# Kernel optimization log

Measured on AMD Instinct MI355X. Metric: run time of the kernel, lower is better.

Reference implementation:

```python
import jax, jax.numpy as jnp
import numpy as np

B, S, H = 2, 2048, 1024
E, K, I = 8, 2, 512
NSH = 2
IS = I * NSH           # shared-expert intermediate = moe_inter * n_shared_experts
NUM_TASKS = 3
TEMP = 1.0             # router_temperature_init (eval: no annealing, no noise)


def setup_inputs() -> dict:
    key = jax.random.key(0)
    ks = jax.random.split(key, 11)
    s_h = 1.0 / np.sqrt(H).astype(np.float32)
    s_i = 1.0 / np.sqrt(I).astype(np.float32)
    s_is = 1.0 / np.sqrt(IS).astype(np.float32)
    return {
        "hidden_states": jax.random.normal(ks[0], (B, S, H), jnp.float32),
        "task_id": 1,
        "gate_w": jax.random.normal(ks[1], (E, H), jnp.float32) * s_h,
        "task_emb": jax.random.normal(ks[2], (NUM_TASKS, H), jnp.float32) * 0.02,
        "We_gate": jax.random.normal(ks[3], (E, H, I), jnp.float32) * s_h,
        "We_up": jax.random.normal(ks[4], (E, H, I), jnp.float32) * s_h,
        "We_down": jax.random.normal(ks[5], (E, I, H), jnp.float32) * s_i,
        "Ws_gate": jax.random.normal(ks[6], (H, IS), jnp.float32) * s_h,
        "Ws_up": jax.random.normal(ks[7], (H, IS), jnp.float32) * s_h,
        "Ws_down": jax.random.normal(ks[8], (IS, H), jnp.float32) * s_is,
        "Wc": jax.random.normal(ks[9], (H, 2), jnp.float32) * s_h,
    }


def _gelu(x):
    return jax.nn.gelu(x, approximate=False)  # matches torch F.gelu default (erf)


def reference(hidden_states, task_id, gate_w, task_emb, We_gate, We_up, We_down,
              Ws_gate, Ws_up, Ws_down, Wc):
    b, s, h = hidden_states.shape
    flat = hidden_states.reshape(-1, h)            # [T, H]
    T = flat.shape[0]

    # ---- NoisyTopKGating (eval: no gumbel noise, no dropout, no aux loss) ----
    gate_in = flat + task_emb[task_id]             # task-conditioned router input
    logits = (gate_in @ gate_w.T) / TEMP           # [T, E]
    scores = jax.nn.softmax(logits, axis=-1)
    topk_w, topk_idx = jax.lax.top_k(scores, K)    # [T, K]
    topk_w = topk_w / (topk_w.sum(-1, keepdims=True) + 1e-20)  # norm_topk_prob

    # dense combine weights [T, E]: zero except the top-k routed experts
    w_dense = jnp.zeros((T, E), scores.dtype).at[
        jnp.arange(T)[:, None], topk_idx].set(topk_w)

    # ---- routed experts: gated MLP per expert, weighted scatter-combine ----
    g = _gelu(jnp.einsum('td,edi->eti', flat, We_gate))   # [E, T, I]
    u = jnp.einsum('td,edi->eti', flat, We_up)            # [E, T, I]
    local = jnp.einsum('eti,te,eid->td', g * u, w_dense, We_down)
    local = local.reshape(b, s, h)

    # ---- shared expert (wider gated MLP over all tokens) ----
    shared = (_gelu(hidden_states @ Ws_gate) * (hidden_states @ Ws_up)) @ Ws_down

    # ---- combination gate: softmax over (local, shared) ----
    alpha = jax.nn.softmax(hidden_states @ Wc, axis=-1)   # [B, S, 2]
    return alpha[..., 0:1] * local + alpha[..., 1:2] * shared
```

## Files before the change

kernel.cpp:

```cpp
#include <hip/hip_runtime.h>
#include <hip/hip_bf16.h>


typedef short  s16x8 __attribute__((ext_vector_type(8)));
typedef __bf16 bf16x8 __attribute__((ext_vector_type(8)));
typedef float  f32x4 __attribute__((ext_vector_type(4)));

__device__ __forceinline__ float b2f(ushort u) {
  union { unsigned int i; float f; } v; v.i = ((unsigned int)u) << 16; return v.f;
}
__device__ __forceinline__ ushort f2b(float f) {
  union { float f; unsigned int i; } v; v.f = f;
  unsigned int r = v.i + 0x7fffu + ((v.i >> 16) & 1u);
  return (ushort)(r >> 16);
}
__device__ __forceinline__ f32x4 mfma_bf16(s16x8 a, s16x8 b, f32x4 c) {
  return __builtin_amdgcn_mfma_f32_16x16x32_bf16(
      __builtin_bit_cast(bf16x8, a), __builtin_bit_cast(bf16x8, b), c, 0, 0, 0);
}
__device__ __forceinline__ void gll16(const ushort* g, const ushort* l) {
  __builtin_amdgcn_global_load_lds(
      (const __attribute__((address_space(1))) unsigned int*)g,
      (__attribute__((address_space(3))) unsigned int*)l, 16, 0, 0);
}

__global__ __launch_bounds__(256) void prep_k(
    const float* __restrict__ X, const float* __restrict__ Gw,
    const float* __restrict__ Temb, const int* __restrict__ task_id,
    const float* __restrict__ Wc,
    const float* __restrict__ Weg, const float* __restrict__ Weu,
    const float* __restrict__ Wed, const float* __restrict__ Wsg,
    const float* __restrict__ Wsu, const float* __restrict__ Wsd,
    ushort* __restrict__ GT, ushort* __restrict__ UT, ushort* __restrict__ DT,
    float* __restrict__ scales, int* __restrict__ topk,
    ushort* __restrict__ Xb)
{
  const int id = blockIdx.x;
  if (id < 15360) {
    const float* src; ushort* dst; int srcLd, dstLd, c0, r0;
    if (id < 8192) {
      int z = id >> 9, rem = id & 511;
      src = (z < 8 ? Weg + (size_t)z * 512 * 1024 : Weu + (size_t)(z - 8) * 512 * 1024);
      dst = (z < 8 ? GT + (size_t)z * 512 * 1024 : UT + (size_t)(z - 8) * 512 * 1024);
      srcLd = 512; dstLd = 1024;
      c0 = (rem & 15) * 32; r0 = (rem >> 4) * 32;
    } else if (id < 12288) {
      int id2 = id - 8192, z = id2 >> 9, rem = id2 & 511;
      src = Wed + (size_t)z * 512 * 1024; dst = DT + (size_t)z * 512;
      srcLd = 1024; dstLd = 5120;
      c0 = (rem & 31) * 32; r0 = (rem >> 5) * 32;
    } else {
      int id3 = id - 12288, z = id3 >> 10, rem = id3 & 1023;
      src = (z == 0 ? Wsg : z == 1 ? Wsu : Wsd);
      dst = (z == 0 ? GT + 4096 * 1024 : z == 1 ? UT + 4096 * 1024 : DT + 4096);
      srcLd = 1024; dstLd = (z == 2 ? 5120 : 1024);
      c0 = (rem & 31) * 32; r0 = (rem >> 5) * 32;
    }
    __shared__ float tile[32][33];
    const int tx = threadIdx.x & 31, ty = threadIdx.x >> 5;
#pragma unroll
    for (int j = 0; j < 4; ++j)
      tile[ty + j * 8][tx] = src[(size_t)(r0 + ty + j * 8) * srcLd + c0 + tx];
    __syncthreads();
#pragma unroll
    for (int j = 0; j < 4; ++j)
      dst[(size_t)(c0 + ty + j * 8) * dstLd + r0 + tx] = f2b(tile[tx][ty + j * 8]);
    return;
  }

  const int rid = id - 15360;
  const int wid = threadIdx.x >> 6, lane = threadIdx.x & 63;
  const int t = rid * 4 + wid;
  const float* xr = X + t * 1024;
  const float* er = Temb + task_id[0] * 1024;

  float x[16], xe[16];
#pragma unroll
  for (int c = 0; c < 4; ++c) {
    float4 v = *(const float4*)&xr[c * 256 + lane * 4];
    float4 e = *(const float4*)&er[c * 256 + lane * 4];
    x[c * 4 + 0] = v.x; x[c * 4 + 1] = v.y; x[c * 4 + 2] = v.z; x[c * 4 + 3] = v.w;
    xe[c * 4 + 0] = v.x + e.x; xe[c * 4 + 1] = v.y + e.y;
    xe[c * 4 + 2] = v.z + e.z; xe[c * 4 + 3] = v.w + e.w;
  }
#pragma unroll
  for (int c = 0; c < 4; ++c) {
    ushort4 o;
    o.x = f2b(x[c * 4 + 0]); o.y = f2b(x[c * 4 + 1]);
    o.z = f2b(x[c * 4 + 2]); o.w = f2b(x[c * 4 + 3]);
    *(ushort4*)&Xb[t * 1024 + c * 256 + lane * 4] = o;
  }
  float logit[8];
#pragma unroll
  for (int e = 0; e < 8; ++e) {
    float p = 0.f;
#pragma unroll
    for (int c = 0; c < 4; ++c) {
      float4 g = *(const float4*)&Gw[e * 1024 + c * 256 + lane * 4];
      p += xe[c * 4] * g.x + xe[c * 4 + 1] * g.y + xe[c * 4 + 2] * g.z + xe[c * 4 + 3] * g.w;
    }
#pragma unroll
    for (int off = 32; off; off >>= 1) p += __shfl_xor(p, off);
    logit[e] = p;
  }
  float m = logit[0];
#pragma unroll
  for (int e = 1; e < 8; ++e) m = fmaxf(m, logit[e]);
  float pr[8], s = 0.f;
#pragma unroll
  for (int e = 0; e < 8; ++e) { pr[e] = expf(logit[e] - m); s += pr[e]; }
  float inv = 1.f / s;
#pragma unroll
  for (int e = 0; e < 8; ++e) pr[e] *= inv;
  int i1 = 0; float m1 = pr[0];
#pragma unroll
  for (int e = 1; e < 8; ++e) if (pr[e] > m1) { m1 = pr[e]; i1 = e; }
  int i2 = -1; float m2 = -1.f;
#pragma unroll
  for (int e = 0; e < 8; ++e) if (e != i1 && pr[e] > m2) { m2 = pr[e]; i2 = e; }
  float dn = 1.f / (m1 + m2 + 1e-20f);
  float w1 = m1 * dn, w2 = m2 * dn;

  float a0 = 0.f, a1 = 0.f;
#pragma unroll
  for (int c = 0; c < 4; ++c)
#pragma unroll
    for (int j = 0; j < 4; ++j) {
      int h = c * 256 + lane * 4 + j;
      a0 += x[c * 4 + j] * Wc[h * 2];
      a1 += x[c * 4 + j] * Wc[h * 2 + 1];
    }
#pragma unroll
  for (int off = 32; off; off >>= 1) {
    a0 += __shfl_xor(a0, off); a1 += __shfl_xor(a1, off);
  }
  float am = fmaxf(a0, a1);
  float ea0 = expf(a0 - am), ea1 = expf(a1 - am);
  float al0 = ea0 / (ea0 + ea1), al1 = ea1 / (ea0 + ea1);

  if (lane == 0) {
    scales[t * 4 + 0] = al0 * w1;
    scales[t * 4 + 1] = al0 * w2;
    scales[t * 4 + 2] = al1;
    topk[t * 2 + 0] = i1;
    topk[t * 2 + 1] = i2;
  }
}

__global__ __launch_bounds__(256) void indexbuild_k(
    const int* __restrict__ topk, const float* __restrict__ scales,
    int* __restrict__ tokmap, int* __restrict__ tokrows,
    float* __restrict__ rowscale, int* __restrict__ meta)
{
  __shared__ int cnt[8], cnt2[8], base[8];
  const int tid = threadIdx.x;
  if (tid < 8) { cnt[tid] = 0; cnt2[tid] = 0; }
  __syncthreads();
  for (int t = tid; t < 4096; t += 256) {
    atomicAdd(&cnt[topk[t * 2]], 1);
    atomicAdd(&cnt[topk[t * 2 + 1]], 1);
  }
  __syncthreads();
  if (tid == 0) {
    int nb128 = 0, nb64 = 0;
    for (int e = 0; e < 8; ++e) {
      base[e] = nb128 * 128;
      int b128 = (cnt[e] + 127) >> 7;
      for (int j = 0; j < b128; ++j) meta[320 + nb128 + j] = e;
      int b64 = (cnt[e] + 63) >> 6;
      for (int j = 0; j < b64; ++j) {
        meta[nb64 + j] = e;
        meta[160 + nb64 + j] = base[e] + j * 64;
      }
      nb128 += b128; nb64 += b64;
    }
    meta[510] = nb64; meta[511] = nb128;
  }
  __syncthreads();
  for (int t = tid; t < 4096; t += 256) {
#pragma unroll
    for (int r = 0; r < 2; ++r) {
      int e = topk[t * 2 + r];
      int slot = atomicAdd(&cnt2[e], 1);
      int row = base[e] + slot;
      tokmap[row] = t;
      rowscale[row] = scales[t * 4 + r];
      tokrows[t * 2 + r] = row;
    }
  }
  __syncthreads();
  for (int e = 0; e < 8; ++e) {
    int c = cnt[e], R = ((c + 63) >> 6) << 6;
    for (int j = c + tid; j < R; j += 256) {
      tokmap[base[e] + j] = 0;
      rowscale[base[e] + j] = 0.f;
    }
  }
}

__global__ __launch_bounds__(256) void gemm1_k(
    const ushort* __restrict__ Xb, const ushort* __restrict__ GT,
    const ushort* __restrict__ UT, const float* __restrict__ scales,
    const int* __restrict__ tokmap, const float* __restrict__ rowscale,
    const int* __restrict__ meta, ushort* __restrict__ Bg,
    ushort* __restrict__ Bs)
{
  __shared__ __align__(16) ushort lA[64 * 64];
  __shared__ __align__(16) ushort lG[64 * 64];
  __shared__ __align__(16) ushort lU[64 * 64];
  const int x = blockIdx.x, y = blockIdx.y;
  const bool routed = y < 144;
  if (routed && (x >= 8 || y >= meta[510])) return;

  const int tid = threadIdx.x, wid = tid >> 6, lane = tid & 63;
  const int col0 = x * 64;
  const int row0 = routed ? meta[160 + y] : (y - 144) * 64;
  const int colG = routed ? (meta[y] * 512 + col0) : (4096 + col0);
  const int wr = (wid >> 1) * 32, wc = (wid & 1) * 32;
  ushort* __restrict__ Out = routed ? Bg : Bs;
  const int outLd = routed ? 512 : 1024;

  int aOff[2], gOff[2], ldsO[2];
#pragma unroll
  for (int i = 0; i < 2; ++i) {
    int q = i * 256 + tid;
    int r = q >> 3, c = q & 7, lc = c ^ (r & 7);
    int arow = routed ? tokmap[row0 + r] : (row0 + r);
    aOff[i] = arow * 1024 + lc * 8;
    gOff[i] = (colG + r) * 1024 + lc * 8;
    ldsO[i] = (i * 256 + (tid & ~63)) * 8;
  }

  f32x4 accG[2][2] = {};
  f32x4 accU[2][2] = {};
  for (int k0 = 0; k0 < 1024; k0 += 64) {
    if (k0) __syncthreads();
#pragma unroll
    for (int i = 0; i < 2; ++i) gll16(Xb + aOff[i] + k0, lA + ldsO[i]);
#pragma unroll
    for (int i = 0; i < 2; ++i) gll16(GT + gOff[i] + k0, lG + ldsO[i]);
#pragma unroll
    for (int i = 0; i < 2; ++i) gll16(UT + gOff[i] + k0, lU + ldsO[i]);
    __syncthreads();
#pragma unroll
    for (int kc = 0; kc < 2; ++kc) {
      const int clog = kc * 4 + (lane >> 4);
      s16x8 af[2], gf[2], uf[2];
#pragma unroll
      for (int fr = 0; fr < 2; ++fr) {
        int rl = wr + fr * 16 + (lane & 15);
        af[fr] = *(const s16x8*)&lA[rl * 64 + ((clog ^ (rl & 7)) << 3)];
      }
#pragma unroll
      for (int cf = 0; cf < 2; ++cf) {
        int cl = wc + cf * 16 + (lane & 15);
        int off = cl * 64 + ((clog ^ (cl & 7)) << 3);
        gf[cf] = *(const s16x8*)&lG[off];
        uf[cf] = *(const s16x8*)&lU[off];
      }
#pragma unroll
      for (int fr = 0; fr < 2; ++fr)
#pragma unroll
        for (int cf = 0; cf < 2; ++cf) {
          accG[fr][cf] = mfma_bf16(af[fr], gf[cf], accG[fr][cf]);
          accU[fr][cf] = mfma_bf16(af[fr], uf[cf], accU[fr][cf]);
        }
    }
  }
#pragma unroll
  for (int fr = 0; fr < 2; ++fr)
#pragma unroll
    for (int r = 0; r < 4; ++r) {
      const int row = row0 + wr + fr * 16 + ((lane >> 4) << 2) + r;
      const float sc = routed ? rowscale[row] : scales[row * 4 + 2];
#pragma unroll
      for (int cf = 0; cf < 2; ++cf) {
        const int col = col0 + wc + cf * 16 + (lane & 15);
        float g = accG[fr][cf][r];
        float u = accU[fr][cf][r];
        float a = 0.5f * g * (1.0f + erff(g * 0.70710678118654752f));
        Out[(size_t)row * outLd + col] = f2b(a * u * sc);
      }
    }
}

template<int ROUTED>
__global__ __launch_bounds__(256) void gemm2_k(
    const ushort* __restrict__ A, const ushort* __restrict__ DT,
    const int* __restrict__ meta, const int* __restrict__ tokrows,
    const ushort* __restrict__ Rrows, ushort* __restrict__ OutB,
    float* __restrict__ OutF)
{
  __shared__ __align__(16) ushort lA[128 * 64];
  __shared__ __align__(16) ushort lB[128 * 64];
  int e = 0;
  if (ROUTED) {
    if ((int)blockIdx.y >= meta[511]) return;
    e = meta[320 + blockIdx.y];
  }
  const int K = ROUTED ? 512 : 1024;
  const int bBase = ROUTED ? e * 512 : 4096;
  const int tid = threadIdx.x, wid = tid >> 6, lane = tid & 63;
  const int col0 = blockIdx.x * 128, row0 = blockIdx.y * 128;
  const int wr = (wid >> 1) * 64, wc = (wid & 1) * 64;

  int aOff[4], bOff[4], lds[4];
#pragma unroll
  for (int i = 0; i < 4; ++i) {
    int q = i * 256 + tid;
    int r = q >> 3, c = q & 7, lc = c ^ (r & 7);
    aOff[i] = (row0 + r) * K + lc * 8;
    bOff[i] = (col0 + r) * 5120 + bBase + lc * 8;
    lds[i]  = (i * 256 + (tid & ~63)) * 8;
  }
  f32x4 acc[4][4] = {};
  for (int k0 = 0; k0 < K; k0 += 64) {
    if (k0) __syncthreads();
#pragma unroll
    for (int i = 0; i < 4; ++i) gll16(A + aOff[i] + k0, lA + lds[i]);
#pragma unroll
    for (int i = 0; i < 4; ++i) gll16(DT + bOff[i] + k0, lB + lds[i]);
    __syncthreads();
#pragma unroll
    for (int kc = 0; kc < 2; ++kc) {
      const int clog = kc * 4 + (lane >> 4);
      s16x8 af[4], bf[4];
#pragma unroll
      for (int fr = 0; fr < 4; ++fr) {
        int rl = wr + fr * 16 + (lane & 15);
        af[fr] = *(const s16x8*)&lA[rl * 64 + ((clog ^ (rl & 7)) << 3)];
      }
#pragma unroll
      for (int cf = 0; cf < 4; ++cf) {
        int cl = wc + cf * 16 + (lane & 15);
        bf[cf] = *(const s16x8*)&lB[cl * 64 + ((clog ^ (cl & 7)) << 3)];
      }
#pragma unroll
      for (int fr = 0; fr < 4; ++fr)
#pragma unroll
        for (int cf = 0; cf < 4; ++cf)
          acc[fr][cf] = mfma_bf16(af[fr], bf[cf], acc[fr][cf]);
    }
  }
#pragma unroll
  for (int fr = 0; fr < 4; ++fr)
#pragma unroll
    for (int r = 0; r < 4; ++r) {
      const int row = row0 + wr + fr * 16 + ((lane >> 4) << 2) + r;
      if (ROUTED) {
#pragma unroll
        for (int cf = 0; cf < 4; ++cf) {
          const int col = col0 + wc + cf * 16 + (lane & 15);
          OutB[row * 1024 + col] = f2b(acc[fr][cf][r]);
        }
      } else {
        const int r0 = tokrows[row * 2], r1 = tokrows[row * 2 + 1];
#pragma unroll
        for (int cf = 0; cf < 4; ++cf) {
          const int col = col0 + wc + cf * 16 + (lane & 15);
          float v = acc[fr][cf][r]
                  + b2f(Rrows[r0 * 1024 + col]) + b2f(Rrows[r1 * 1024 + col]);
          OutF[row * 1024 + col] = v;
        }
      }
    }
}

extern "C" void kernel_launch(void* const* d_in, const int* in_sizes, int n_in,
                              void* d_out, int out_size, void* d_ws, size_t ws_size,
                              hipStream_t stream) {
  const float* X    = (const float*)d_in[0];
  const int*   task = (const int*)  d_in[1];
  const float* Gw   = (const float*)d_in[2];
  const float* Temb = (const float*)d_in[3];
  const float* Weg  = (const float*)d_in[4];
  const float* Weu  = (const float*)d_in[5];
  const float* Wed  = (const float*)d_in[6];
  const float* Wsg  = (const float*)d_in[7];
  const float* Wsu  = (const float*)d_in[8];
  const float* Wsd  = (const float*)d_in[9];
  const float* Wc   = (const float*)d_in[10];

  char* ws = (char*)d_ws;
  float*  scales   = (float*)(ws + 0x00000);
  int*    topk     = (int*)  (ws + 0x10000);
  int*    tokmap   = (int*)  (ws + 0x18000);
  int*    tokrows  = (int*)  (ws + 0x22000);
  float*  rowscale = (float*)(ws + 0x2A000);
  int*    meta     = (int*)  (ws + 0x34000);
  ushort* Xb       = (ushort*)(ws + 0x40000);
  ushort* GT       = Xb + 4096 * 1024;
  ushort* UT       = GT + 5120 * 1024;
  ushort* DT       = UT + 5120 * 1024;
  ushort* Bg       = DT + 1024 * 5120;
  ushort* Bs       = Bg + 9216 * 512;
  ushort* out_r    = Bs + 4096 * 1024;

  prep_k<<<16384, 256, 0, stream>>>(X, Gw, Temb, task, Wc,
                                    Weg, Weu, Wed, Wsg, Wsu, Wsd,
                                    GT, UT, DT, scales, topk, Xb);
  indexbuild_k<<<1, 256, 0, stream>>>(topk, scales, tokmap, tokrows, rowscale, meta);

  gemm1_k<<<dim3(16, 208), 256, 0, stream>>>(Xb, GT, UT, scales, tokmap, rowscale, meta, Bg, Bs);

  gemm2_k<1><<<dim3(8, 72), 256, 0, stream>>>(Bg, DT, meta, tokrows, (const ushort*)nullptr, out_r, (float*)nullptr);
  gemm2_k<0><<<dim3(8, 32), 256, 0, stream>>>(Bs, DT, meta, tokrows, out_r, (ushort*)nullptr, (float*)d_out);
}
```

Baseline: 175.3 us.

## Split prep kernel into transpose/router launches and swizzle GEMM block order

Splits the monolithic prep kernel into three templated transpose kernels plus a separate router kernel, removing the branchy block-id decoding. Remaps the blockIdx.y order in gemm1 and gemm2 so that consecutive blocks are spread across row tiles, meant to improve cache locality or spread work evenly across XCDs. Padding to 128 rows in indexbuild is also widened. The extra launches add launch overhead, and the y-permutation must stay a bijection over the grid.

```diff
diff --git a/kernel.cpp b/kernel.cpp
--- a/kernel.cpp
+++ b/kernel.cpp
@@ -24,53 +24,46 @@
       (__attribute__((address_space(3))) unsigned int*)l, 16, 0, 0);
 }
 
-__global__ __launch_bounds__(256) void prep_k(
+template<int MODE>
+__global__ __launch_bounds__(256) void transpose_k(
+    const float* __restrict__ S0, const float* __restrict__ S1,
+    const float* __restrict__ S2, ushort* __restrict__ D0,
+    ushort* __restrict__ D1, ushort* __restrict__ D2)
+{
+  const int z = blockIdx.z;
+  const float* src; ushort* dst; int srcLd, dstLd;
+  if (MODE == 0) {
+    src = (z < 8 ? S0 + (size_t)z * 512 * 1024 : S1 + (size_t)(z - 8) * 512 * 1024);
+    dst = (z < 8 ? D0 + (size_t)z * 512 * 1024 : D1 + (size_t)(z - 8) * 512 * 1024);
+    srcLd = 512; dstLd = 1024;
+  } else if (MODE == 1) {
+    src = S0 + (size_t)z * 512 * 1024; dst = D0 + (size_t)z * 512;
+    srcLd = 1024; dstLd = 5120;
+  } else {
+    src = (z == 0 ? S0 : z == 1 ? S1 : S2);
+    dst = (z == 0 ? D0 : z == 1 ? D1 : D2);
+    srcLd = 1024; dstLd = (z == 2 ? 5120 : 1024);
+  }
+  __shared__ float tile[32][33];
+  const int c0 = blockIdx.x * 32, r0 = blockIdx.y * 32;
+  const int tx = threadIdx.x & 31, ty = threadIdx.x >> 5;
+#pragma unroll
+  for (int j = 0; j < 4; ++j)
+    tile[ty + j * 8][tx] = src[(size_t)(r0 + ty + j * 8) * srcLd + c0 + tx];
+  __syncthreads();
+#pragma unroll
+  for (int j = 0; j < 4; ++j)
+    dst[(size_t)(c0 + ty + j * 8) * dstLd + r0 + tx] = f2b(tile[tx][ty + j * 8]);
+}
+
+__global__ __launch_bounds__(256) void router_k(
     const float* __restrict__ X, const float* __restrict__ Gw,
     const float* __restrict__ Temb, const int* __restrict__ task_id,
-    const float* __restrict__ Wc,
-    const float* __restrict__ Weg, const float* __restrict__ Weu,
-    const float* __restrict__ Wed, const float* __restrict__ Wsg,
-    const float* __restrict__ Wsu, const float* __restrict__ Wsd,
-    ushort* __restrict__ GT, ushort* __restrict__ UT, ushort* __restrict__ DT,
-    float* __restrict__ scales, int* __restrict__ topk,
-    ushort* __restrict__ Xb)
+    const float* __restrict__ Wc, float* __restrict__ scales,
+    int* __restrict__ topk, ushort* __restrict__ Xb)
 {
-  const int id = blockIdx.x;
-  if (id < 15360) {
-    const float* src; ushort* dst; int srcLd, dstLd, c0, r0;
-    if (id < 8192) {
-      int z = id >> 9, rem = id & 511;
-      src = (z < 8 ? Weg + (size_t)z * 512 * 1024 : Weu + (size_t)(z - 8) * 512 * 1024);
-      dst = (z < 8 ? GT + (size_t)z * 512 * 1024 : UT + (size_t)(z - 8) * 512 * 1024);
-      srcLd = 512; dstLd = 1024;
-      c0 = (rem & 15) * 32; r0 = (rem >> 4) * 32;
-    } else if (id < 12288) {
-      int id2 = id - 8192, z = id2 >> 9, rem = id2 & 511;
-      src = Wed + (size_t)z * 512 * 1024; dst = DT + (size_t)z * 512;
-      srcLd = 1024; dstLd = 5120;
-      c0 = (rem & 31) * 32; r0 = (rem >> 5) * 32;
-    } else {
-      int id3 = id - 12288, z = id3 >> 10, rem = id3 & 1023;
-      src = (z == 0 ? Wsg : z == 1 ? Wsu : Wsd);
-      dst = (z == 0 ? GT + 4096 * 1024 : z == 1 ? UT + 4096 * 1024 : DT + 4096);
-      srcLd = 1024; dstLd = (z == 2 ? 5120 : 1024);
-      c0 = (rem & 31) * 32; r0 = (rem >> 5) * 32;
-    }
-    __shared__ float tile[32][33];
-    const int tx = threadIdx.x & 31, ty = threadIdx.x >> 5;
-#pragma unroll
-    for (int j = 0; j < 4; ++j)
-      tile[ty + j * 8][tx] = src[(size_t)(r0 + ty + j * 8) * srcLd + c0 + tx];
-    __syncthreads();
-#pragma unroll
-    for (int j = 0; j < 4; ++j)
-      dst[(size_t)(c0 + ty + j * 8) * dstLd + r0 + tx] = f2b(tile[tx][ty + j * 8]);
-    return;
-  }
-
-  const int rid = id - 15360;
   const int wid = threadIdx.x >> 6, lane = threadIdx.x & 63;
-  const int t = rid * 4 + wid;
+  const int t = blockIdx.x * 4 + wid;
   const float* xr = X + t * 1024;
   const float* er = Temb + task_id[0] * 1024;
 
@@ -190,7 +183,7 @@
   }
   __syncthreads();
   for (int e = 0; e < 8; ++e) {
-    int c = cnt[e], R = ((c + 63) >> 6) << 6;
+    int c = cnt[e], R = ((c + 127) >> 7) << 7;
     for (int j = c + tid; j < R; j += 256) {
       tokmap[base[e] + j] = 0;
       rowscale[base[e] + j] = 0.f;
@@ -210,12 +203,14 @@
   __shared__ __align__(16) ushort lU[64 * 64];
   const int x = blockIdx.x, y = blockIdx.y;
   const bool routed = y < 144;
-  if (routed && (x >= 8 || y >= meta[510])) return;
+  const int ys = routed ? ((y & 7) * 18 + (y >> 3))
+                        : (((y - 144) & 7) * 8 + ((y - 144) >> 3));
+  if (routed && (x >= 8 || ys >= meta[510])) return;
 
   const int tid = threadIdx.x, wid = tid >> 6, lane = tid & 63;
   const int col0 = x * 64;
-  const int row0 = routed ? meta[160 + y] : (y - 144) * 64;
-  const int colG = routed ? (meta[y] * 512 + col0) : (4096 + col0);
+  const int row0 = routed ? meta[160 + ys] : ys * 64;
+  const int colG = routed ? (meta[ys] * 512 + col0) : (4096 + col0);
   const int wr = (wid >> 1) * 32, wc = (wid & 1) * 32;
   ushort* __restrict__ Out = routed ? Bg : Bs;
   const int outLd = routed ? 512 : 1024;
@@ -293,15 +288,18 @@
 {
   __shared__ __align__(16) ushort lA[128 * 64];
   __shared__ __align__(16) ushort lB[128 * 64];
+  const int yraw = blockIdx.y;
+  const int ys = ROUTED ? ((yraw & 7) * 9 + (yraw >> 3))
+                        : ((yraw & 7) * 4 + (yraw >> 3));
   int e = 0;
   if (ROUTED) {
-    if ((int)blockIdx.y >= meta[511]) return;
-    e = meta[320 + blockIdx.y];
+    if (ys >= meta[511]) return;
+    e = meta[320 + ys];
   }
   const int K = ROUTED ? 512 : 1024;
   const int bBase = ROUTED ? e * 512 : 4096;
   const int tid = threadIdx.x, wid = tid >> 6, lane = tid & 63;
-  const int col0 = blockIdx.x * 128, row0 = blockIdx.y * 128;
+  const int col0 = blockIdx.x * 128, row0 = ys * 128;
   const int wr = (wid >> 1) * 64, wc = (wid & 1) * 64;
 
   int aOff[4], bOff[4], lds[4];
@@ -396,9 +394,12 @@
   ushort* Bs       = Bg + 9216 * 512;
   ushort* out_r    = Bs + 4096 * 1024;
 
-  prep_k<<<16384, 256, 0, stream>>>(X, Gw, Temb, task, Wc,
-                                    Weg, Weu, Wed, Wsg, Wsu, Wsd,
-                                    GT, UT, DT, scales, topk, Xb);
+  transpose_k<0><<<dim3(16, 32, 16), 256, 0, stream>>>(Weg, Weu, nullptr, GT, UT, nullptr);
+  transpose_k<1><<<dim3(32, 16, 8), 256, 0, stream>>>(Wed, nullptr, nullptr, DT, nullptr, nullptr);
+  transpose_k<2><<<dim3(32, 32, 3), 256, 0, stream>>>(
+      Wsg, Wsu, Wsd, GT + 4096 * 1024, UT + 4096 * 1024, DT + 4096);
+
+  router_k<<<1024, 256, 0, stream>>>(X, Gw, Temb, task, Wc, scales, topk, Xb);
   indexbuild_k<<<1, 256, 0, stream>>>(topk, scales, tokmap, tokrows, rowscale, meta);
 
   gemm1_k<<<dim3(16, 208), 256, 0, stream>>>(Xb, GT, UT, scales, tokmap, rowscale, meta, Bg, Bs);
```

Result: slower. 179.2 us (+2.2%).
